# Kernel optimization log

Hardware: AMD Instinct MI355X
Metric: run time of the kernel (lower is better)

Reference implementation:

```python
import jax, jax.numpy as jnp
import numpy as np

EMBED = 1536
HEADS = 12
EPS = 1e-5


def _layernorm(x, gamma, beta):
    mu = x.mean(axis=-1, keepdims=True)
    var = ((x - mu) ** 2).mean(axis=-1, keepdims=True)
    return (x - mu) * jax.lax.rsqrt(var + EPS) * gamma + beta


def setup_inputs() -> dict:
    key = jax.random.key(0)
    ks = jax.random.split(key, 8)
    N, L, E = 8, 2048, EMBED
    x = jax.random.normal(ks[0], (N, L, E), dtype=jnp.float32)
    s = 0.02
    Wv = jax.random.normal(ks[1], (E, E), dtype=jnp.float32) * s
    Wk = jax.random.normal(ks[2], (E, E), dtype=jnp.float32) * s
    Wq = jax.random.normal(ks[3], (E, E), dtype=jnp.float32) * s
    Wo = jax.random.normal(ks[4], (E, E), dtype=jnp.float32) * s
    bo = jnp.zeros((E,), dtype=jnp.float32)
    gamma = jnp.ones((E,), dtype=jnp.float32)
    beta = jnp.zeros((E,), dtype=jnp.float32)
    return {"combined_embeddings": x, "Wv": Wv, "Wk": Wk, "Wq": Wq,
            "Wo": Wo, "bo": bo, "gamma": gamma, "beta": beta}


def reference(combined_embeddings, Wv, Wk, Wq, Wo, bo, gamma, beta):
    x = combined_embeddings
    N, L, E = x.shape
    H, hd = HEADS, E // HEADS
    # projections (torch Linear: x @ W^T), reshape to (N, H, L, hd)
    v = (x @ Wv.T).reshape(N, L, H, hd).transpose(0, 2, 1, 3)
    k = (x @ Wk.T).reshape(N, L, H, hd).transpose(0, 2, 1, 3)
    q = (x @ Wq.T).reshape(N, L, H, hd).transpose(0, 2, 1, 3)
    # NOTE: faithful to the source, einsum labels treat axis1 (heads) as q/k
    # and axis2 (sequence) as h -> heads-over-heads attention per position.
    energy = jnp.einsum('nqhd,nkhd->nhqk', q, k)  # (N, L, H, H)
    attention = jax.nn.softmax(energy / jnp.sqrt(jnp.float32(E)), axis=3)
    out = jnp.einsum('nhql,nlhd->nqhd', attention, v)  # (N, H, L, hd)
    out = out.transpose(0, 2, 1, 3).reshape(N, L, E)
    out = out @ Wo.T + bo
    out = _layernorm(out + x, gamma, beta)
    # small extra attention
    e_actions = out[:, 2:][None]          # (1, N, L-2, E)
    e_state = out.mean(axis=1)[None]      # (1, N, E)
    scores = jnp.matmul(e_state, jnp.swapaxes(e_actions, -2, -1))
    scores = scores / jnp.sqrt(jnp.float32(E))   # (1, N, N, L-2)
    weights = jax.nn.softmax(scores, axis=-1)
    attended = jnp.matmul(weights, e_actions)    # (1, N, N, E)
    return attended, weights
```

## Files before the change

### kernel.cpp

```cpp
#include <hip/hip_runtime.h>
#include <stdint.h>

typedef unsigned short u16;
typedef __bf16 bf16_t;
typedef bf16_t bf16x8 __attribute__((ext_vector_type(8)));
typedef float f32x4 __attribute__((ext_vector_type(4)));

#define E_DIM 1536
#define N_B 8
#define L_SEQ 2048
#define NT 2046
#define SCALE 0.025515518f
#define LN_EPS 1e-5f
#define NTILES 24

__device__ __forceinline__ u16 f2b(float f) {
  union { float f; uint32_t u; } v; v.f = f;
  uint32_t u = v.u + 0x7FFFu + ((v.u >> 16) & 1u);
  return (u16)(u >> 16);
}
__device__ __forceinline__ float b2f(u16 h) {
  union { uint32_t u; float f; } v; v.u = ((uint32_t)h) << 16; return v.f;
}

__device__ __forceinline__ void gload16(const u16* g, const bf16_t* l) {
  __builtin_amdgcn_global_load_lds((const __attribute__((address_space(1))) void*)g,
                                   (__attribute__((address_space(3))) void*)l,
                                   16, 0, 0);
}

#define BAR()   __builtin_amdgcn_s_barrier()
#define SCHB()  __builtin_amdgcn_sched_barrier(0)
#define VM4()   asm volatile("s_waitcnt vmcnt(4)" ::: "memory")
#define VM0()   asm volatile("s_waitcnt vmcnt(0)" ::: "memory")

__global__ void cvt_kernel(const float* __restrict__ in, u16* __restrict__ out, int nvec) {
  int i = blockIdx.x * 256 + threadIdx.x;
  if (i < nvec) {
    float4 f = ((const float4*)in)[i];
    ushort4 u;
    u.x = f2b(f.x); u.y = f2b(f.y); u.z = f2b(f.z); u.w = f2b(f.w);
    ((ushort4*)out)[i] = u;
  }
}

template<int FUSED>
__launch_bounds__(512, 2)
__global__ void gemm2c(const u16* __restrict__ Ag,
                       const u16* __restrict__ B0w, const u16* __restrict__ B1w,
                       const u16* __restrict__ B2w,
                       u16* __restrict__ C0, u16* __restrict__ C1, u16* __restrict__ C2,
                       float* __restrict__ Cf, const float* __restrict__ bias,
                       const float* __restrict__ resid)
{
  extern __shared__ __attribute__((aligned(16))) bf16_t lds[];

  const int flat = (blockIdx.z * gridDim.y + blockIdx.y) * gridDim.x + blockIdx.x;
  const int xcd = flat & 7, bb_ = flat >> 3;
  const int gl = bb_ / 24, jj = bb_ % 24;
  const int g = gl * 8 + xcd;
  const int zz = g >> 4;
  const int gy = g & 15;
  const int tx = jj >> 2;
  const int ty = gy * 4 + (jj & 3);
  const int rowA = ty * 256, colB = tx * 256;

  const u16* Bg; u16* Cb;
  if (zz == 0)      { Bg = B0w; Cb = C0; }
  else if (zz == 1) { Bg = B1w; Cb = C1; }
  else              { Bg = B2w; Cb = C2; }

  const int tid = threadIdx.x;
  const int w = tid >> 6, lane = tid & 63;
  const int wr = w >> 2, wc = w & 3;

  const int rl = lane & 15, lsl = lane >> 4;
  const int sw8 = (lsl ^ ((rl >> 1) & 3)) * 8;
  const int arow = (wr * 128 + rl) * 32 + sw8;
  const int brow = (wc * 64 + rl) * 32 + sw8;

  const int r0s = tid >> 2, sps = tid & 3;
  const int sws = (sps ^ ((r0s >> 1) & 3)) * 8;
  const size_t sA0 = (size_t)(rowA + r0s) * E_DIM + sws;
  const size_t sA1 = (size_t)(rowA + 128 + r0s) * E_DIM + sws;
  const size_t sB0 = (size_t)(colB + r0s) * E_DIM + sws;
  const size_t sB1 = (size_t)(colB + 128 + r0s) * E_DIM + sws;
  const int wb0 = w * 512, wb1 = 4096 + w * 512;

  f32x4 acc[8][4];
#pragma unroll
  for (int m = 0; m < 8; ++m)
#pragma unroll
    for (int n = 0; n < 4; ++n)
#pragma unroll
      for (int q = 0; q < 4; ++q) acc[m][n][q] = 0.0f;

  gload16(Ag + sA0,      lds + 0     + wb0);  gload16(Ag + sA1,      lds + 0     + wb1);
  gload16(Bg + sB0,      lds + 32768 + wb0);  gload16(Bg + sB1,      lds + 32768 + wb1);
  gload16(Ag + sA0 + 32, lds + 8192  + wb0);  gload16(Ag + sA1 + 32, lds + 8192  + wb1);
  gload16(Bg + sB0 + 32, lds + 40960 + wb0);  gload16(Bg + sB1 + 32, lds + 40960 + wb1);
  gload16(Ag + sA0 + 64, lds + 16384 + wb0);  gload16(Ag + sA1 + 64, lds + 16384 + wb1);
  gload16(Bg + sB0 + 64, lds + 49152 + wb0);  gload16(Bg + sB1 + 64, lds + 49152 + wb1);
  VM4();
  BAR();

  bf16x8 a0[8], b0[4], a1[8], b1[4];
#pragma unroll
  for (int m = 0; m < 8; ++m) a0[m] = *(const bf16x8*)&lds[0 + arow + m * 512];
#pragma unroll
  for (int n = 0; n < 4; ++n) b0[n] = *(const bf16x8*)&lds[32768 + brow + n * 512];

  for (int t = 0; t < NTILES; ++t) {
    const int cur = t & 1, nxt = cur ^ 1;
    const int Ak1 = (cur * 2 + 1) * 8192, Bk1 = 32768 + (cur * 2 + 1) * 8192;
    const int AkN0 = nxt * 2 * 8192,      BkN0 = 32768 + nxt * 2 * 8192;
    const int AkN1 = (nxt * 2 + 1) * 8192, BkN1 = 32768 + (nxt * 2 + 1) * 8192;

#pragma unroll
    for (int m = 0; m < 8; ++m) a1[m] = *(const bf16x8*)&lds[Ak1 + arow + m * 512];
#pragma unroll
    for (int n = 0; n < 4; ++n) b1[n] = *(const bf16x8*)&lds[Bk1 + brow + n * 512];
    if (t + 1 < NTILES) {
      const size_t ko = (size_t)(t + 1) * 64 + 32;
      gload16(Ag + sA0 + ko, lds + AkN1 + wb0);  gload16(Ag + sA1 + ko, lds + AkN1 + wb1);
      gload16(Bg + sB0 + ko, lds + BkN1 + wb0);  gload16(Bg + sB1 + ko, lds + BkN1 + wb1);
    }
    SCHB();
    __builtin_amdgcn_s_setprio(1);
#pragma unroll
    for (int m = 0; m < 8; ++m)
#pragma unroll
      for (int n = 0; n < 4; ++n)
        acc[m][n] = __builtin_amdgcn_mfma_f32_16x16x32_bf16(a0[m], b0[n], acc[m][n], 0, 0, 0);
    __builtin_amdgcn_s_setprio(0);
    SCHB();
    if (t + 1 < NTILES) { VM4(); }
    BAR();

    if (t + 2 < NTILES) {
      const size_t ko = (size_t)(t + 2) * 64;
      gload16(Ag + sA0 + ko, lds + cur * 2 * 8192 + wb0);
      gload16(Ag + sA1 + ko, lds + cur * 2 * 8192 + wb1);
      gload16(Bg + sB0 + ko, lds + 32768 + cur * 2 * 8192 + wb0);
      gload16(Bg + sB1 + ko, lds + 32768 + cur * 2 * 8192 + wb1);
    }
    if (t + 1 < NTILES) {
#pragma unroll
      for (int m = 0; m < 8; ++m) a0[m] = *(const bf16x8*)&lds[AkN0 + arow + m * 512];
#pragma unroll
      for (int n = 0; n < 4; ++n) b0[n] = *(const bf16x8*)&lds[BkN0 + brow + n * 512];
    }
    SCHB();
    __builtin_amdgcn_s_setprio(1);
#pragma unroll
    for (int m = 0; m < 8; ++m)
#pragma unroll
      for (int n = 0; n < 4; ++n)
        acc[m][n] = __builtin_amdgcn_mfma_f32_16x16x32_bf16(a1[m], b1[n], acc[m][n], 0, 0, 0);
    __builtin_amdgcn_s_setprio(0);
    SCHB();
    if (t + 2 < NTILES)      { VM4(); }
    else if (t + 1 < NTILES) { VM0(); }
    BAR();
  }

  const int r0 = (lane >> 4) * 4;
#pragma unroll
  for (int m = 0; m < 8; ++m) {
#pragma unroll
    for (int n = 0; n < 4; ++n) {
      const int gcol = colB + wc * 64 + n * 16 + rl;
#pragma unroll
      for (int q = 0; q < 4; ++q) {
        const int grow = rowA + wr * 128 + m * 16 + r0 + q;
        const size_t idx = (size_t)grow * E_DIM + gcol;
        if (FUSED) Cf[idx] = acc[m][n][q] + bias[gcol] + resid[idx];
        else       Cb[idx] = f2b(acc[m][n][q]);
      }
    }
  }
}

__launch_bounds__(256)
__global__ void headmix(const u16* __restrict__ qb, const u16* __restrict__ kb,
                        const u16* __restrict__ vb, u16* __restrict__ aob)
{
  __shared__ float qs[12 * 132], ks2[12 * 132], vs[12 * 132];
  __shared__ float att[12][12];
  const int tid = threadIdx.x;
  const size_t base = (size_t)blockIdx.x * E_DIM;

  for (int e = tid; e < E_DIM; e += 256) {
    int i = e >> 7, d = e & 127, p = i * 132 + d;
    qs[p]  = b2f(qb[base + e]);
    ks2[p] = b2f(kb[base + e]);
    vs[p]  = b2f(vb[base + e]);
  }
  __syncthreads();

  if (tid < 144) {
    int i = tid / 12, j = tid % 12;
    float s = 0.f;
#pragma unroll 8
    for (int d = 0; d < 128; ++d) s += qs[i * 132 + d] * ks2[j * 132 + d];
    att[i][j] = s * SCALE;
  }
  __syncthreads();

  if (tid < 12) {
    float mx = att[tid][0];
#pragma unroll
    for (int j = 1; j < 12; ++j) mx = fmaxf(mx, att[tid][j]);
    float ev[12], sum = 0.f;
#pragma unroll
    for (int j = 0; j < 12; ++j) { ev[j] = expf(att[tid][j] - mx); sum += ev[j]; }
    float inv = 1.f / sum;
#pragma unroll
    for (int j = 0; j < 12; ++j) att[tid][j] = ev[j] * inv;
  }
  __syncthreads();

  for (int e = tid; e < E_DIM; e += 256) {
    int i = e >> 7, d = e & 127;
    float o = 0.f;
#pragma unroll
    for (int j = 0; j < 12; ++j) o += att[i][j] * vs[j * 132 + d];
    aob[base + e] = f2b(o);
  }
}

__launch_bounds__(256)
__global__ void ln_kernel(float* __restrict__ p, const float* __restrict__ gamma,
                          const float* __restrict__ beta)
{
  __shared__ float rs[4], rq[4];
  __shared__ float mean_s, rstd_s;
  const int tid = threadIdx.x, w = tid >> 6, lane = tid & 63;
  float* row = p + (size_t)blockIdx.x * E_DIM;

  float v[6], s = 0.f, sq = 0.f;
#pragma unroll
  for (int i = 0; i < 6; ++i) {
    v[i] = row[tid + i * 256];
    s += v[i]; sq += v[i] * v[i];
  }
#pragma unroll
  for (int off = 32; off > 0; off >>= 1) {
    s  += __shfl_down(s, off);
    sq += __shfl_down(sq, off);
  }
  if (lane == 0) { rs[w] = s; rq[w] = sq; }
  __syncthreads();
  if (tid == 0) {
    float S = rs[0] + rs[1] + rs[2] + rs[3];
    float Q = rq[0] + rq[1] + rq[2] + rq[3];
    float mu = S * (1.f / 1536.f);
    float var = Q * (1.f / 1536.f) - mu * mu;
    mean_s = mu; rstd_s = rsqrtf(var + LN_EPS);
  }
  __syncthreads();
  const float mu = mean_s, rstd = rstd_s;
#pragma unroll
  for (int i = 0; i < 6; ++i) {
    int e = tid + i * 256;
    row[e] = (v[i] - mu) * rstd * gamma[e] + beta[e];
  }
}

__global__ void estate_partial(const float* __restrict__ outp, float* __restrict__ part)
{
  const int e = blockIdx.x * 256 + threadIdx.x;
  const int b = blockIdx.y, z = blockIdx.z;
  const float* p = outp + ((size_t)b * L_SEQ + z * 256) * E_DIM + e;
  float acc = 0.f;
  for (int l = 0; l < 256; ++l) acc += p[(size_t)l * E_DIM];
  part[(size_t)(z * N_B + b) * E_DIM + e] = acc;
}
__global__ void estate_reduce(const float* __restrict__ part, float* __restrict__ est)
{
  const int i = blockIdx.x * 256 + threadIdx.x;
  if (i < N_B * E_DIM) {
    float s = 0.f;
#pragma unroll
    for (int z = 0; z < 8; ++z) s += part[(size_t)z * N_B * E_DIM + i];
    est[i] = s * (1.f / 2048.f);
  }
}

__launch_bounds__(256)
__global__ void scores_kernel(const float* __restrict__ outp, const float* __restrict__ est,
                              float* __restrict__ wout)
{
  __shared__ float es[N_B * E_DIM];
  const int tid = threadIdx.x, wv = tid >> 6, lane = tid & 63;
  const int b = blockIdx.y;
  for (int i = tid; i < N_B * E_DIM; i += 256) es[i] = est[i];
  __syncthreads();

  for (int ti = 0; ti < 16; ++ti) {
    int t = blockIdx.x * 64 + wv * 16 + ti;
    if (t >= NT) continue;
    const float* row = outp + ((size_t)b * L_SEQ + 2 + t) * E_DIM;
    float a[8];
#pragma unroll
    for (int s = 0; s < 8; ++s) a[s] = 0.f;
    for (int c = 0; c < 24; ++c) {
      int idx = c * 64 + lane;
      float val = row[idx];
#pragma unroll
      for (int s = 0; s < 8; ++s) a[s] += es[s * E_DIM + idx] * val;
    }
#pragma unroll
    for (int off = 32; off > 0; off >>= 1)
#pragma unroll
      for (int s = 0; s < 8; ++s) a[s] += __shfl_down(a[s], off);
    if (lane == 0) {
#pragma unroll
      for (int s = 0; s < 8; ++s)
        wout[(size_t)(b * N_B + s) * NT + t] = a[s] * SCALE;
    }
  }
}

__launch_bounds__(256)
__global__ void softmax_w(float* __restrict__ wbase)
{
  float* p = wbase + (size_t)blockIdx.x * NT;
  __shared__ float r1[4], r2[4];
  __shared__ float bmax, bsum;
  const int tid = threadIdx.x, wv = tid >> 6, lane = tid & 63;

  float vals[8], mx = -1e30f;
#pragma unroll
  for (int i = 0; i < 8; ++i) {
    int t = tid + i * 256;
    vals[i] = (t < NT) ? p[t] : -1e30f;
    mx = fmaxf(mx, vals[i]);
  }
#pragma unroll
  for (int off = 32; off > 0; off >>= 1) mx = fmaxf(mx, __shfl_down(mx, off));
  if (lane == 0) r1[wv] = mx;
  __syncthreads();
  if (tid == 0) bmax = fmaxf(fmaxf(r1[0], r1[1]), fmaxf(r1[2], r1[3]));
  __syncthreads();
  mx = bmax;

  float sum = 0.f;
#pragma unroll
  for (int i = 0; i < 8; ++i) {
    int t = tid + i * 256;
    if (t < NT) { vals[i] = expf(vals[i] - mx); sum += vals[i]; }
  }
#pragma unroll
  for (int off = 32; off > 0; off >>= 1) sum += __shfl_down(sum, off);
  if (lane == 0) r2[wv] = sum;
  __syncthreads();
  if (tid == 0) bsum = r2[0] + r2[1] + r2[2] + r2[3];
  __syncthreads();
  const float inv = 1.f / bsum;
#pragma unroll
  for (int i = 0; i < 8; ++i) {
    int t = tid + i * 256;
    if (t < NT) p[t] = vals[i] * inv;
  }
}

__launch_bounds__(256)
__global__ void attended_partial(const float* __restrict__ outp, const float* __restrict__ wts,
                                 float* __restrict__ part)
{
  const int tid = threadIdx.x;
  const int e = blockIdx.x * 256 + tid;
  const int b = blockIdx.y, z = blockIdx.z;
  __shared__ float wl[8][256];
  float a[8];
#pragma unroll
  for (int s = 0; s < 8; ++s) a[s] = 0.f;

  const int tbeg = z * 512;
  const int tend = (tbeg + 512 < NT) ? tbeg + 512 : NT;
  for (int tb = tbeg; tb < tend; tb += 256) {
    const int cnt = (tend - tb < 256) ? (tend - tb) : 256;
    __syncthreads();
    for (int i = tid; i < 8 * 256; i += 256) {
      int s = i >> 8, tt = i & 255;
      wl[s][tt] = (tt < cnt) ? wts[(size_t)(b * N_B + s) * NT + tb + tt] : 0.f;
    }
    __syncthreads();
    for (int tt = 0; tt < cnt; ++tt) {
      float val = outp[((size_t)b * L_SEQ + 2 + tb + tt) * E_DIM + e];
#pragma unroll
      for (int s = 0; s < 8; ++s) a[s] += wl[s][tt] * val;
    }
  }
#pragma unroll
  for (int s = 0; s < 8; ++s)
    part[(((size_t)z * N_B + b) * N_B + s) * E_DIM + e] = a[s];
}
__global__ void attended_reduce(const float* __restrict__ part, float* __restrict__ outp)
{
  const int i = blockIdx.x * 256 + threadIdx.x;
  float s = 0.f;
#pragma unroll
  for (int z = 0; z < 4; ++z) s += part[(size_t)z * N_B * N_B * E_DIM + i];
  outp[i] = s;
}

extern "C" void kernel_launch(void* const* d_in, const int* in_sizes, int n_in,
                              void* d_out, int out_size, void* d_ws, size_t ws_size,
                              hipStream_t stream)
{
  (void)in_sizes; (void)n_in; (void)out_size; (void)ws_size;
  const float* x     = (const float*)d_in[0];
  const float* Wv    = (const float*)d_in[1];
  const float* Wk    = (const float*)d_in[2];
  const float* Wq    = (const float*)d_in[3];
  const float* Wo    = (const float*)d_in[4];
  const float* bo    = (const float*)d_in[5];
  const float* gamma = (const float*)d_in[6];
  const float* beta  = (const float*)d_in[7];
  float* out = (float*)d_out;

  char* ws = (char*)d_ws;
  size_t off = 0;
  auto alloc = [&](size_t bytes) -> void* {
    void* p = ws + off;
    off += (bytes + 255) & ~(size_t)255;
    return p;
  };
  const size_t ME = (size_t)16384 * E_DIM;
  const size_t WE = (size_t)E_DIM * E_DIM;
  u16*   xb    = (u16*)alloc(ME * 2);
  u16*   wqb   = (u16*)alloc(WE * 2);
  u16*   wkb   = (u16*)alloc(WE * 2);
  u16*   wvb   = (u16*)alloc(WE * 2);
  u16*   wob   = (u16*)alloc(WE * 2);
  u16*   qb    = (u16*)alloc(ME * 2);
  u16*   kb    = (u16*)alloc(ME * 2);
  u16*   vb    = (u16*)alloc(ME * 2);
  u16*   aob   = (u16*)alloc(ME * 2);
  float* lnbuf = (float*)alloc(ME * 4);
  float* est   = (float*)alloc((size_t)N_B * E_DIM * 4);
  float* estp  = (float*)alloc((size_t)8 * N_B * E_DIM * 4);
  float* attp  = (float*)alloc((size_t)4 * N_B * N_B * E_DIM * 4);

  float* wout = out + 98304;

  hipFuncSetAttribute(reinterpret_cast<const void*>(gemm2c<0>),
                      hipFuncAttributeMaxDynamicSharedMemorySize, 131072);
  hipFuncSetAttribute(reinterpret_cast<const void*>(gemm2c<1>),
                      hipFuncAttributeMaxDynamicSharedMemorySize, 131072);

  cvt_kernel<<<dim3((6291456 + 255) / 256), 256, 0, stream>>>(x, xb, 6291456);
  cvt_kernel<<<dim3((589824 + 255) / 256), 256, 0, stream>>>(Wq, wqb, 589824);
  cvt_kernel<<<dim3((589824 + 255) / 256), 256, 0, stream>>>(Wk, wkb, 589824);
  cvt_kernel<<<dim3((589824 + 255) / 256), 256, 0, stream>>>(Wv, wvb, 589824);
  cvt_kernel<<<dim3((589824 + 255) / 256), 256, 0, stream>>>(Wo, wob, 589824);

  gemm2c<0><<<dim3(6, 64, 3), 512, 131072, stream>>>(
      xb, wqb, wkb, wvb, qb, kb, vb, nullptr, nullptr, nullptr);

  headmix<<<dim3(16384), 256, 0, stream>>>(qb, kb, vb, aob);

  gemm2c<1><<<dim3(6, 64, 1), 512, 131072, stream>>>(
      aob, wob, wob, wob, nullptr, nullptr, nullptr, lnbuf, bo, x);

  ln_kernel<<<dim3(16384), 256, 0, stream>>>(lnbuf, gamma, beta);

  estate_partial<<<dim3(6, 8, 8), 256, 0, stream>>>(lnbuf, estp);
  estate_reduce<<<dim3(48), 256, 0, stream>>>(estp, est);

  scores_kernel<<<dim3(32, 8), 256, 0, stream>>>(lnbuf, est, wout);
  softmax_w<<<dim3(64), 256, 0, stream>>>(wout);

  attended_partial<<<dim3(6, 8, 4), 256, 0, stream>>>(lnbuf, wout, attp);
  attended_reduce<<<dim3(384), 256, 0, stream>>>(attp, out);
}
```

Baseline: 567.8 us.

## Restructure GEMM main loop into 4-slot ring with half-tile LDS/MFMA interleave

Replaces the double-buffered 64-wide K loop with a 4-slot ring of 32-wide K stages, splitting each stage's MFMA work into two M-halves. LDS reads for the next half are issued before the current half's MFMAs and gated by explicit lgkmcnt waits, with global prefetch running three stages ahead. The aim is to hide LDS-read and global-load latency behind matrix instructions with fewer live fragment registers. It adds more barriers per K step and a hand-written tail schedule whose wait counts must stay correct.

```diff
diff --git a/kernel.cpp b/kernel.cpp
--- a/kernel.cpp
+++ b/kernel.cpp
@@ -12,7 +12,6 @@
 #define NT 2046
 #define SCALE 0.025515518f
 #define LN_EPS 1e-5f
-#define NTILES 24
 
 __device__ __forceinline__ u16 f2b(float f) {
   union { float f; uint32_t u; } v; v.f = f;
@@ -31,6 +30,10 @@
 
 #define BAR()   __builtin_amdgcn_s_barrier()
 #define SCHB()  __builtin_amdgcn_sched_barrier(0)
+#define LG0()   asm volatile("s_waitcnt lgkmcnt(0)" ::: "memory")
+#define LG4()   asm volatile("s_waitcnt lgkmcnt(4)" ::: "memory")
+#define LG8()   asm volatile("s_waitcnt lgkmcnt(8)" ::: "memory")
+#define VM8()   asm volatile("s_waitcnt vmcnt(8)" ::: "memory")
 #define VM4()   asm volatile("s_waitcnt vmcnt(4)" ::: "memory")
 #define VM0()   asm volatile("s_waitcnt vmcnt(0)" ::: "memory")
 
@@ -46,12 +49,12 @@
 
 template<int FUSED>
 __launch_bounds__(512, 2)
-__global__ void gemm2c(const u16* __restrict__ Ag,
-                       const u16* __restrict__ B0w, const u16* __restrict__ B1w,
-                       const u16* __restrict__ B2w,
-                       u16* __restrict__ C0, u16* __restrict__ C1, u16* __restrict__ C2,
-                       float* __restrict__ Cf, const float* __restrict__ bias,
-                       const float* __restrict__ resid)
+__global__ void gemml(const u16* __restrict__ Ag,
+                      const u16* __restrict__ B0w, const u16* __restrict__ B1w,
+                      const u16* __restrict__ B2w,
+                      u16* __restrict__ C0, u16* __restrict__ C1, u16* __restrict__ C2,
+                      float* __restrict__ Cf, const float* __restrict__ bias,
+                      const float* __restrict__ resid)
 {
   extern __shared__ __attribute__((aligned(16))) bf16_t lds[];
 
@@ -95,74 +98,62 @@
 #pragma unroll
       for (int q = 0; q < 4; ++q) acc[m][n][q] = 0.0f;
 
-  gload16(Ag + sA0,      lds + 0     + wb0);  gload16(Ag + sA1,      lds + 0     + wb1);
-  gload16(Bg + sB0,      lds + 32768 + wb0);  gload16(Bg + sB1,      lds + 32768 + wb1);
-  gload16(Ag + sA0 + 32, lds + 8192  + wb0);  gload16(Ag + sA1 + 32, lds + 8192  + wb1);
-  gload16(Bg + sB0 + 32, lds + 40960 + wb0);  gload16(Bg + sB1 + 32, lds + 40960 + wb1);
-  gload16(Ag + sA0 + 64, lds + 16384 + wb0);  gload16(Ag + sA1 + 64, lds + 16384 + wb1);
-  gload16(Bg + sB0 + 64, lds + 49152 + wb0);  gload16(Bg + sB1 + 64, lds + 49152 + wb1);
-  VM4();
+  bf16x8 aC[4], aN[4], bC[4], bN[4];
+
+  auto stageU = [&](int un, int slot) {
+    const size_t ko = (size_t)un * 32;
+    bf16_t* dA = lds + slot * 8192;
+    bf16_t* dB = lds + 32768 + slot * 8192;
+    gload16(Ag + sA0 + ko, dA + wb0);
+    gload16(Ag + sA1 + ko, dA + wb1);
+    gload16(Bg + sB0 + ko, dB + wb0);
+    gload16(Bg + sB1 + ko, dB + wb1);
+  };
+  auto rdA = [&](bf16x8 (&d)[4], int slot, int mh) {
+#pragma unroll
+    for (int i = 0; i < 4; ++i)
+      d[i] = *(const bf16x8*)&lds[slot * 8192 + arow + (mh * 4 + i) * 512];
+  };
+  auto rdB = [&](bf16x8 (&d)[4], int slot) {
+#pragma unroll
+    for (int n = 0; n < 4; ++n)
+      d[n] = *(const bf16x8*)&lds[32768 + slot * 8192 + brow + n * 512];
+  };
+  auto mf = [&](const bf16x8 (&a)[4], const bf16x8 (&b)[4], int mh) {
+    __builtin_amdgcn_s_setprio(1);
+#pragma unroll
+    for (int i = 0; i < 4; ++i)
+#pragma unroll
+      for (int n = 0; n < 4; ++n)
+        acc[mh * 4 + i][n] =
+            __builtin_amdgcn_mfma_f32_16x16x32_bf16(a[i], b[n], acc[mh * 4 + i][n], 0, 0, 0);
+    __builtin_amdgcn_s_setprio(0);
+  };
+
+  stageU(0, 0); stageU(1, 1); stageU(2, 2);
+  VM8();
   BAR();
-
-  bf16x8 a0[8], b0[4], a1[8], b1[4];
-#pragma unroll
-  for (int m = 0; m < 8; ++m) a0[m] = *(const bf16x8*)&lds[0 + arow + m * 512];
-#pragma unroll
-  for (int n = 0; n < 4; ++n) b0[n] = *(const bf16x8*)&lds[32768 + brow + n * 512];
-
-  for (int t = 0; t < NTILES; ++t) {
-    const int cur = t & 1, nxt = cur ^ 1;
-    const int Ak1 = (cur * 2 + 1) * 8192, Bk1 = 32768 + (cur * 2 + 1) * 8192;
-    const int AkN0 = nxt * 2 * 8192,      BkN0 = 32768 + nxt * 2 * 8192;
-    const int AkN1 = (nxt * 2 + 1) * 8192, BkN1 = 32768 + (nxt * 2 + 1) * 8192;
-
-#pragma unroll
-    for (int m = 0; m < 8; ++m) a1[m] = *(const bf16x8*)&lds[Ak1 + arow + m * 512];
-#pragma unroll
-    for (int n = 0; n < 4; ++n) b1[n] = *(const bf16x8*)&lds[Bk1 + brow + n * 512];
-    if (t + 1 < NTILES) {
-      const size_t ko = (size_t)(t + 1) * 64 + 32;
-      gload16(Ag + sA0 + ko, lds + AkN1 + wb0);  gload16(Ag + sA1 + ko, lds + AkN1 + wb1);
-      gload16(Bg + sB0 + ko, lds + BkN1 + wb0);  gload16(Bg + sB1 + ko, lds + BkN1 + wb1);
-    }
-    SCHB();
-    __builtin_amdgcn_s_setprio(1);
-#pragma unroll
-    for (int m = 0; m < 8; ++m)
-#pragma unroll
-      for (int n = 0; n < 4; ++n)
-        acc[m][n] = __builtin_amdgcn_mfma_f32_16x16x32_bf16(a0[m], b0[n], acc[m][n], 0, 0, 0);
-    __builtin_amdgcn_s_setprio(0);
-    SCHB();
-    if (t + 1 < NTILES) { VM4(); }
-    BAR();
-
-    if (t + 2 < NTILES) {
-      const size_t ko = (size_t)(t + 2) * 64;
-      gload16(Ag + sA0 + ko, lds + cur * 2 * 8192 + wb0);
-      gload16(Ag + sA1 + ko, lds + cur * 2 * 8192 + wb1);
-      gload16(Bg + sB0 + ko, lds + 32768 + cur * 2 * 8192 + wb0);
-      gload16(Bg + sB1 + ko, lds + 32768 + cur * 2 * 8192 + wb1);
-    }
-    if (t + 1 < NTILES) {
-#pragma unroll
-      for (int m = 0; m < 8; ++m) a0[m] = *(const bf16x8*)&lds[AkN0 + arow + m * 512];
-#pragma unroll
-      for (int n = 0; n < 4; ++n) b0[n] = *(const bf16x8*)&lds[BkN0 + brow + n * 512];
-    }
-    SCHB();
-    __builtin_amdgcn_s_setprio(1);
-#pragma unroll
-    for (int m = 0; m < 8; ++m)
-#pragma unroll
-      for (int n = 0; n < 4; ++n)
-        acc[m][n] = __builtin_amdgcn_mfma_f32_16x16x32_bf16(a1[m], b1[n], acc[m][n], 0, 0, 0);
-    __builtin_amdgcn_s_setprio(0);
-    SCHB();
-    if (t + 2 < NTILES)      { VM4(); }
-    else if (t + 1 < NTILES) { VM0(); }
-    BAR();
-  }
+  rdA(aC, 0, 0); rdB(bC, 0);
+
+  for (int tt = 0; tt < 11; ++tt) {
+    const int u3 = 4 * tt + 3, u4 = u3 + 1, u5 = u3 + 2, u6 = u3 + 3;
+    rdA(aN, 0, 1);              stageU(u3, 3);  BAR(); LG4(); SCHB(); mf(aC, bC, 0); VM8(); BAR();
+    rdA(aC, 1, 0); rdB(bN, 1);                  BAR(); LG8(); SCHB(); mf(aN, bC, 1);        BAR();
+    rdA(aN, 1, 1);              stageU(u4, 0);  BAR(); LG4(); SCHB(); mf(aC, bN, 0); VM8(); BAR();
+    rdA(aC, 2, 0); rdB(bC, 2);                  BAR(); LG8(); SCHB(); mf(aN, bN, 1);        BAR();
+    rdA(aN, 2, 1);              stageU(u5, 1);  BAR(); LG4(); SCHB(); mf(aC, bC, 0); VM8(); BAR();
+    rdA(aC, 3, 0); rdB(bN, 3);                  BAR(); LG8(); SCHB(); mf(aN, bC, 1);        BAR();
+    rdA(aN, 3, 1);              stageU(u6, 2);  BAR(); LG4(); SCHB(); mf(aC, bN, 0); VM8(); BAR();
+    rdA(aC, 0, 0); rdB(bC, 0);                  BAR(); LG8(); SCHB(); mf(aN, bN, 1);        BAR();
+  }
+  rdA(aN, 0, 1);                stageU(47, 3);  BAR(); LG4(); SCHB(); mf(aC, bC, 0); VM8(); BAR();
+  rdA(aC, 1, 0); rdB(bN, 1);                    BAR(); LG8(); SCHB(); mf(aN, bC, 1);        BAR();
+  rdA(aN, 1, 1);                                BAR(); LG4(); SCHB(); mf(aC, bN, 0); VM4(); BAR();
+  rdA(aC, 2, 0); rdB(bC, 2);                    BAR(); LG8(); SCHB(); mf(aN, bN, 1);        BAR();
+  rdA(aN, 2, 1);                                BAR(); LG4(); SCHB(); mf(aC, bC, 0); VM0(); BAR();
+  rdA(aC, 3, 0); rdB(bN, 3);                    BAR(); LG8(); SCHB(); mf(aN, bC, 1);        BAR();
+  rdA(aN, 3, 1);                                BAR(); LG4(); SCHB(); mf(aC, bN, 0);        BAR();
+                                                BAR(); LG0(); SCHB(); mf(aN, bN, 1);
 
   const int r0 = (lane >> 4) * 4;
 #pragma unroll
@@ -446,9 +437,9 @@
 
   float* wout = out + 98304;
 
-  hipFuncSetAttribute(reinterpret_cast<const void*>(gemm2c<0>),
+  hipFuncSetAttribute(reinterpret_cast<const void*>(gemml<0>),
                       hipFuncAttributeMaxDynamicSharedMemorySize, 131072);
-  hipFuncSetAttribute(reinterpret_cast<const void*>(gemm2c<1>),
+  hipFuncSetAttribute(reinterpret_cast<const void*>(gemml<1>),
                       hipFuncAttributeMaxDynamicSharedMemorySize, 131072);
 
   cvt_kernel<<<dim3((6291456 + 255) / 256), 256, 0, stream>>>(x, xb, 6291456);
@@ -457,12 +448,12 @@
   cvt_kernel<<<dim3((589824 + 255) / 256), 256, 0, stream>>>(Wv, wvb, 589824);
   cvt_kernel<<<dim3((589824 + 255) / 256), 256, 0, stream>>>(Wo, wob, 589824);
 
-  gemm2c<0><<<dim3(6, 64, 3), 512, 131072, stream>>>(
+  gemml<0><<<dim3(6, 64, 3), 512, 131072, stream>>>(
       xb, wqb, wkb, wvb, qb, kb, vb, nullptr, nullptr, nullptr);
 
   headmix<<<dim3(16384), 256, 0, stream>>>(qb, kb, vb, aob);
 
-  gemm2c<1><<<dim3(6, 64, 1), 512, 131072, stream>>>(
+  gemml<1><<<dim3(6, 64, 1), 512, 131072, stream>>>(
       aob, wob, wob, wob, nullptr, nullptr, nullptr, lnbuf, bo, x);
 
   ln_kernel<<<dim3(16384), 256, 0, stream>>>(lnbuf, gamma, beta);
```

After: 586.2 us. 3.2% more time.
